# Optimization experiments

Measured on AMD Instinct MI355X. Metric: run time of the kernel, lower is better.

Reference implementation:

```python
import jax, jax.numpy as jnp
import numpy as np

B, S, D = 2, 2048, 2048
H, KVH, DH = 32, 8, 64
G = H // KVH  # num_key_value_groups
SCALE = DH ** -0.5
NEG = -1e9


def rotate_half(x):
    x1, x2 = jnp.split(x, 2, axis=-1)
    return jnp.concatenate([-x2, x1], axis=-1)


def setup_inputs() -> dict:
    key = jax.random.key(0)
    ks = jax.random.split(key, 6)
    hidden_states = jax.random.normal(ks[0], (B, S, D), dtype=jnp.float32)
    # RoPE tables (base 10000), shape [B, S, DH]
    inv_freq = 1.0 / (10000.0 ** (np.arange(0, DH, 2, dtype=np.float32) / DH))
    t = np.arange(S, dtype=np.float32)
    freqs = np.outer(t, inv_freq)                     # [S, DH/2]
    emb = np.concatenate([freqs, freqs], axis=-1)     # [S, DH]
    cos = jnp.broadcast_to(jnp.cos(emb)[None], (B, S, DH)).astype(jnp.float32)
    sin = jnp.broadcast_to(jnp.sin(emb)[None], (B, S, DH)).astype(jnp.float32)
    # additive causal mask [B, 1, S, S]
    causal = np.tril(np.ones((S, S), dtype=bool))
    mask = jnp.asarray(np.where(causal, 0.0, NEG).astype(np.float32))
    attention_mask = jnp.broadcast_to(mask[None, None], (B, 1, S, S))
    std = 0.02
    Wq = jax.random.normal(ks[1], (H * DH, D), dtype=jnp.float32) * std
    Wk = jax.random.normal(ks[2], (KVH * DH, D), dtype=jnp.float32) * std
    Wv = jax.random.normal(ks[3], (KVH * DH, D), dtype=jnp.float32) * std
    Wo = jax.random.normal(ks[4], (D, H * DH), dtype=jnp.float32) * std
    return {"hidden_states": hidden_states, "cos": cos, "sin": sin,
            "attention_mask": attention_mask, "Wq": Wq, "Wk": Wk, "Wv": Wv, "Wo": Wo}


def reference(hidden_states, cos, sin, attention_mask, Wq, Wk, Wv, Wo):
    b, s, d = hidden_states.shape
    # projections -> [B, heads, S, DH]
    q = (hidden_states @ Wq.T).reshape(b, s, H, DH).transpose(0, 2, 1, 3)
    k = (hidden_states @ Wk.T).reshape(b, s, KVH, DH).transpose(0, 2, 1, 3)
    v = (hidden_states @ Wv.T).reshape(b, s, KVH, DH).transpose(0, 2, 1, 3)
    # RoPE (unsqueeze_dim=1)
    c = cos[:, None]  # [B,1,S,DH]
    sn = sin[:, None]
    q = q * c + rotate_half(q) * sn
    k = k * c + rotate_half(k) * sn
    # GQA: repeat kv heads
    k = jnp.repeat(k, G, axis=1)
    v = jnp.repeat(v, G, axis=1)
    scores = jnp.einsum("bhqd,bhkd->bhqk", q, k) * SCALE + attention_mask
    attn = jax.nn.softmax(scores.astype(jnp.float32), axis=-1).astype(q.dtype)
    out = jnp.einsum("bhqk,bhkd->bhqd", attn, v)          # [B,H,S,DH]
    out = out.transpose(0, 2, 1, 3).reshape(b, s, H * DH)  # [B,S,H*DH]
    return out @ Wo.T
```

## Files before the change

kernel.cpp:

```cpp
#include <hip/hip_runtime.h>

typedef unsigned short u16;
typedef __attribute__((ext_vector_type(8))) short s16x8;
typedef __attribute__((ext_vector_type(4))) float f32x4;
typedef __attribute__((ext_vector_type(4))) unsigned short u16x4;

#define MFMA16(a, b, c) __builtin_amdgcn_mfma_f32_16x16x32_bf16(a, b, c, 0, 0, 0)

__device__ __forceinline__ u16 f2bf(float f) {
  unsigned u = __builtin_bit_cast(unsigned, f);
  u += 0x7fffu + ((u >> 16) & 1u);
  return (u16)(u >> 16);
}

__device__ __forceinline__ u16 f2bf_fast(float f) {
  return (u16)((__builtin_bit_cast(unsigned, f) + 0x8000u) >> 16);
}

__device__ __forceinline__ void async16(const void* g, void* l) {
  __builtin_amdgcn_global_load_lds(
      (const __attribute__((address_space(1))) void*)g,
      (__attribute__((address_space(3))) void*)l, 16, 0, 0);
}

__device__ __forceinline__ s16x8 ld8(const u16* p) { return *(const s16x8*)p; }

#define PRE 0.18033688011112042f

__global__ __launch_bounds__(256) void cvt_all(
    const float* __restrict__ X, const float* __restrict__ Wq,
    const float* __restrict__ Wk, const float* __restrict__ Wv,
    const float* __restrict__ Wo, u16* __restrict__ out) {
  long e = (long)(blockIdx.x * 256 + threadIdx.x) * 4;
  const float* src;
  if (e < 8388608L) src = X + e;
  else if (e < 12582912L) src = Wq + (e - 8388608L);
  else if (e < 13631488L) src = Wk + (e - 12582912L);
  else if (e < 14680064L) src = Wv + (e - 13631488L);
  else src = Wo + (e - 14680064L);
  float4 v = *(const float4*)src;
  u16x4 o = {f2bf(v.x), f2bf(v.y), f2bf(v.z), f2bf(v.w)};
  *(u16x4*)(out + e) = o;
}

enum { EPI_QKV = 0, EPI_OUT = 1 };

template <int EPI>
__global__ __launch_bounds__(256) void gemm_nt(
    const u16* __restrict__ A, const u16* __restrict__ Bm,
    const float* __restrict__ cosp, const float* __restrict__ sinp,
    u16* __restrict__ Qo, u16* __restrict__ Ko, u16* __restrict__ Vo,
    float* __restrict__ Co, int K) {
  __shared__ u16 SM[16384];
  const int t = threadIdx.x;
  const int lane = t & 63;
  const int w = t >> 6, wm = w >> 1, wn = w & 1;
  const int quad = lane >> 4, c16 = lane & 15;
  const int m0 = blockIdx.y * 128, n0 = blockIdx.x * 128;

  f32x4 acc[4][4];
  const f32x4 zero = {0.f, 0.f, 0.f, 0.f};
#pragma unroll
  for (int i = 0; i < 4; ++i)
#pragma unroll
    for (int j = 0; j < 4; ++j) acc[i][j] = zero;

  const u16* gA[4];
  const u16* gB[4];
#pragma unroll
  for (int p = 0; p < 4; ++p) {
    int c = t + p * 256;
    int r = c >> 3, cc = (c & 7) ^ (r & 7);
    gA[p] = A + (size_t)(m0 + r) * K + cc * 8;
    gB[p] = Bm + (size_t)(n0 + r) * K + cc * 8;
  }

  for (int k0 = 0; k0 < K; k0 += 64) {
    __syncthreads();
#pragma unroll
    for (int p = 0; p < 4; ++p) {
      async16(gA[p], &SM[(t + p * 256) * 8]);
      async16(gB[p], &SM[8192 + (t + p * 256) * 8]);
      gA[p] += 64;
      gB[p] += 64;
    }
    __syncthreads();
#pragma unroll
    for (int c = 0; c < 2; ++c) {
      s16x8 af[4], bfr[4];
#pragma unroll
      for (int i = 0; i < 4; ++i)
        af[i] = ld8(&SM[(wm * 64 + i * 16 + c16) * 64 +
                        (((c * 4 + quad) ^ (c16 & 7)) * 8)]);
#pragma unroll
      for (int j = 0; j < 4; ++j)
        bfr[j] = ld8(&SM[8192 + (wn * 64 + j * 16 + c16) * 64 +
                         (((c * 4 + quad) ^ (c16 & 7)) * 8)]);
#pragma unroll
      for (int i = 0; i < 4; ++i)
#pragma unroll
        for (int j = 0; j < 4; ++j) acc[i][j] = MFMA16(af[i], bfr[j], acc[i][j]);
    }
  }

  if (EPI == EPI_OUT) {
#pragma unroll
    for (int i = 0; i < 4; ++i)
#pragma unroll
      for (int r = 0; r < 4; ++r) {
        int m = m0 + wm * 64 + i * 16 + quad * 4 + r;
        float* dst = Co + (size_t)m * 2048 + n0 + wn * 64 + c16;
#pragma unroll
        for (int j = 0; j < 4; ++j) dst[j * 16] = acc[i][j][r];
      }
  } else if (n0 >= 2560) {
    __syncthreads();
#pragma unroll
    for (int i = 0; i < 4; ++i)
#pragma unroll
      for (int r = 0; r < 4; ++r) {
        int sl = wm * 64 + i * 16 + quad * 4 + r;
#pragma unroll
        for (int j = 0; j < 4; ++j) {
          int dl = wn * 64 + j * 16 + c16;
          SM[dl * 128 + (((sl >> 3) ^ (dl & 15)) * 8) + (sl & 7)] =
              f2bf(acc[i][j][r]);
        }
      }
    __syncthreads();
    int bb = m0 >> 11, m0s = m0 & 2047;
#pragma unroll
    for (int p = 0; p < 8; ++p) {
      int q = p * 256 + t;
      int dl = q >> 4, k = q & 15;
      s16x8 vrow = ld8(&SM[dl * 128 + ((k ^ (dl & 15)) * 8)]);
      int nab = n0 + dl;
      int kvh = (nab - 2560) >> 6, dh = nab & 63;
      *(s16x8*)(Vo + ((size_t)(bb * 8 + kvh) * 64 + dh) * 2048 + m0s + k * 8) =
          vrow;
    }
  } else {
    const int nbase = n0 + wn * 64;
#pragma unroll
    for (int i = 0; i < 4; ++i)
#pragma unroll
      for (int r = 0; r < 4; ++r) {
        int m = m0 + wm * 64 + i * 16 + quad * 4 + r;
        int b = m >> 11, s = m & 2047;
        if (nbase < 2048) {
          int h = nbase >> 6;
          size_t base = ((size_t)(b * 32 + h) * 2048 + s) * 64;
#pragma unroll
          for (int j = 0; j < 2; ++j) {
            int d = j * 16 + c16;
            float v1 = acc[i][j][r], v2 = acc[i][j + 2][r];
            float c1 = cosp[m * 64 + d], s1 = sinp[m * 64 + d];
            float c2 = cosp[m * 64 + d + 32], s2 = sinp[m * 64 + d + 32];
            Qo[base + d] = f2bf((v1 * c1 - v2 * s1) * PRE);
            Qo[base + d + 32] = f2bf((v2 * c2 + v1 * s2) * PRE);
          }
        } else {
          int h = (nbase - 2048) >> 6;
          size_t base = ((size_t)(b * 8 + h) * 2048 + s) * 64;
#pragma unroll
          for (int j = 0; j < 2; ++j) {
            int d = j * 16 + c16;
            float v1 = acc[i][j][r], v2 = acc[i][j + 2][r];
            float c1 = cosp[m * 64 + d], s1 = sinp[m * 64 + d];
            float c2 = cosp[m * 64 + d + 32], s2 = sinp[m * 64 + d + 32];
            Ko[base + d] = f2bf(v1 * c1 - v2 * s1);
            Ko[base + d + 32] = f2bf(v2 * c2 + v1 * s2);
          }
        }
      }
  }
}

__global__ __launch_bounds__(256) void attn(const u16* __restrict__ Q,
                                            const u16* __restrict__ Kg,
                                            const u16* __restrict__ Vg,
                                            u16* __restrict__ O) {
  __shared__ u16 Ks[2][4096];
  __shared__ u16 Vs[2][4096];
  __shared__ u16 Ps[8192];
  const int t = threadIdx.x;
  const int lane = t & 63;
  const int w = t >> 6;
  const int quad = lane >> 4, c16 = lane & 15;
  const int bh = blockIdx.y;
  const int b = bh >> 5, h = bh & 31;
  const int kvh = h >> 2;

  const u16* Qbase = Q + ((size_t)(b * 32 + h) * 2048) * 64;
  const u16* Kbase = Kg + ((size_t)(b * 8 + kvh) * 2048) * 64;
  const u16* Vbase = Vg + ((size_t)(b * 8 + kvh) * 64) * 2048;

  const int sr0 = t >> 3, sc0 = ((t & 7) ^ (sr0 & 7)) * 8;
  const int sr1 = (t + 256) >> 3, sc1 = (((t + 256) & 7) ^ (sr1 & 7)) * 8;

  for (int ph = 0; ph < 2; ++ph) {
    const int qt = ph ? 15 - blockIdx.x : blockIdx.x;
    const int q0 = qt * 128;

    s16x8 qa[2][2];
#pragma unroll
    for (int im = 0; im < 2; ++im)
#pragma unroll
      for (int c = 0; c < 2; ++c)
        qa[im][c] = ld8(Qbase + (size_t)(q0 + w * 32 + im * 16 + c16) * 64 +
                        c * 32 + quad * 8);

    f32x4 oacc[2][4];
    const f32x4 zero = {0.f, 0.f, 0.f, 0.f};
    float lacc[2][4];
#pragma unroll
    for (int im = 0; im < 2; ++im)
#pragma unroll
      for (int r = 0; r < 4; ++r) lacc[im][r] = 0.f;
#pragma unroll
    for (int im = 0; im < 2; ++im)
#pragma unroll
      for (int dt = 0; dt < 4; ++dt) oacc[im][dt] = zero;

    const int nkt = 2 * qt + 2;

    __syncthreads();
    {
      const u16* kg = Kbase + 0 * 4096;
      async16(kg + sr0 * 64 + sc0, &Ks[0][t * 8]);
      async16(kg + sr1 * 64 + sc1, &Ks[0][t * 8 + 2048]);
      async16(Vbase + (size_t)sr0 * 2048 + sc0, &Vs[0][t * 8]);
      async16(Vbase + (size_t)sr1 * 2048 + sc1, &Vs[0][t * 8 + 2048]);
    }

    for (int kt = 0; kt < nkt; ++kt) {
      const int cur = kt & 1;
      __syncthreads();
      if (kt + 1 < nkt) {
        const int nxt = 1 - cur;
        const u16* kg = Kbase + (kt + 1) * 4096;
        async16(kg + sr0 * 64 + sc0, &Ks[nxt][t * 8]);
        async16(kg + sr1 * 64 + sc1, &Ks[nxt][t * 8 + 2048]);
        async16(Vbase + (size_t)sr0 * 2048 + (kt + 1) * 64 + sc0,
                &Vs[nxt][t * 8]);
        async16(Vbase + (size_t)sr1 * 2048 + (kt + 1) * 64 + sc1,
                &Vs[nxt][t * 8 + 2048]);
      }
      const u16* Kb = Ks[cur];
      const u16* Vb = Vs[cur];

#pragma unroll
      for (int im = 0; im < 2; ++im) {
        f32x4 sc[4];
#pragma unroll
        for (int in = 0; in < 4; ++in) sc[in] = zero;
#pragma unroll
        for (int c = 0; c < 2; ++c)
#pragma unroll
          for (int in = 0; in < 4; ++in) {
            s16x8 kf = ld8(&Kb[(in * 16 + c16) * 64 +
                               (((c * 4 + quad) ^ (c16 & 7)) * 8)]);
            sc[in] = MFMA16(qa[im][c], kf, sc[in]);
          }
        const int rbase = q0 + w * 32 + im * 16;
        if (kt * 64 + 63 > rbase) {
#pragma unroll
          for (int in = 0; in < 4; ++in) {
            int kcol = kt * 64 + in * 16 + c16;
#pragma unroll
            for (int r = 0; r < 4; ++r)
              if (kcol > rbase + quad * 4 + r) sc[in][r] = -1e30f;
          }
        }
#pragma unroll
        for (int in = 0; in < 4; ++in)
#pragma unroll
          for (int r = 0; r < 4; ++r) {
            float p = exp2f(sc[in][r]);
            lacc[im][r] += p;
            int row = im * 16 + quad * 4 + r;
            Ps[w * 2048 + row * 64 +
               (((in * 2 + (c16 >> 3)) ^ (row & 7)) * 8) + (c16 & 7)] =
                f2bf_fast(p);
          }
      }

#pragma unroll
      for (int c = 0; c < 2; ++c) {
        const int swz = ((c * 4 + quad) ^ (c16 & 7)) * 8;
        s16x8 pf[2];
#pragma unroll
        for (int im = 0; im < 2; ++im)
          pf[im] = ld8(&Ps[w * 2048 + (im * 16 + c16) * 64 + swz]);
#pragma unroll
        for (int dt = 0; dt < 4; ++dt) {
          s16x8 vf = ld8(&Vb[(dt * 16 + c16) * 64 + swz]);
#pragma unroll
          for (int im = 0; im < 2; ++im)
            oacc[im][dt] = MFMA16(pf[im], vf, oacc[im][dt]);
        }
      }
    }

#pragma unroll
    for (int im = 0; im < 2; ++im) {
      float inv[4];
#pragma unroll
      for (int r = 0; r < 4; ++r) {
        float v = lacc[im][r];
        v += __shfl_xor(v, 1);
        v += __shfl_xor(v, 2);
        v += __shfl_xor(v, 4);
        v += __shfl_xor(v, 8);
        inv[r] = 1.f / v;
      }
#pragma unroll
      for (int dt = 0; dt < 4; ++dt)
#pragma unroll
        for (int r = 0; r < 4; ++r) {
          int s = q0 + w * 32 + im * 16 + quad * 4 + r;
          O[((size_t)(b * 2048 + s)) * 2048 + h * 64 + dt * 16 + c16] =
              f2bf(oacc[im][dt][r] * inv[r]);
        }
    }
  }
}

extern "C" void kernel_launch(void* const* d_in, const int* in_sizes, int n_in,
                              void* d_out, int out_size, void* d_ws,
                              size_t ws_size, hipStream_t stream) {
  const float* X = (const float*)d_in[0];
  const float* cosp = (const float*)d_in[1];
  const float* sinp = (const float*)d_in[2];
  const float* Wq = (const float*)d_in[4];
  const float* Wk = (const float*)d_in[5];
  const float* Wv = (const float*)d_in[6];
  const float* Wo = (const float*)d_in[7];
  float* out = (float*)d_out;

  u16* Xb = (u16*)d_ws;
  u16* Wqkv = Xb + 8388608;
  u16* Wob = Wqkv + 6291456;
  u16* Qr = Wob + 4194304;
  u16* Kr = Qr + 8388608;
  u16* Vt = Kr + 2097152;
  u16* Ob = Vt + 2097152;

  cvt_all<<<18432, 256, 0, stream>>>(X, Wq, Wk, Wv, Wo, Xb);

  gemm_nt<EPI_QKV><<<dim3(24, 32), 256, 0, stream>>>(
      Xb, Wqkv, cosp, sinp, Qr, Kr, Vt, nullptr, 2048);

  attn<<<dim3(8, 64), 256, 0, stream>>>(Qr, Kr, Vt, Ob);

  gemm_nt<EPI_OUT><<<dim3(16, 32), 256, 0, stream>>>(
      Ob, Wob, nullptr, nullptr, nullptr, nullptr, nullptr, out, 2048);
}
```

Before: 354.7 us.

## Double-buffer GEMM LDS tiles with K-step 32 and prefetch next tile

The projection GEMM main loop now uses two LDS buffers with a K-step of 32 instead of a single buffer with a K-step of 64. The global-to-LDS async load of the next tile is issued before the MFMAs on the current tile, which removes one barrier per iteration and overlaps load latency with compute. The LDS layout packs two rows per 64-element line with a new XOR swizzle, and the fragment offsets are precomputed. In exchange there are twice as many loop iterations, each with less compute to hide the loads behind.

```diff
diff --git a/kernel.cpp b/kernel.cpp
--- a/kernel.cpp
+++ b/kernel.cpp
@@ -65,42 +65,61 @@
 #pragma unroll
     for (int j = 0; j < 4; ++j) acc[i][j] = zero;
 
-  const u16* gA[4];
-  const u16* gB[4];
-#pragma unroll
-  for (int p = 0; p < 4; ++p) {
+  const u16* gA[2];
+  const u16* gB[2];
+  int lof[2];
+#pragma unroll
+  for (int p = 0; p < 2; ++p) {
     int c = t + p * 256;
-    int r = c >> 3, cc = (c & 7) ^ (r & 7);
-    gA[p] = A + (size_t)(m0 + r) * K + cc * 8;
-    gB[p] = Bm + (size_t)(n0 + r) * K + cc * 8;
-  }
-
-  for (int k0 = 0; k0 < K; k0 += 64) {
+    int dr = c >> 3, k8 = (c & 7) ^ (dr & 7);
+    int row = 2 * dr + (k8 >> 2), col = (k8 & 3) * 8;
+    gA[p] = A + (size_t)(m0 + row) * K + col;
+    gB[p] = Bm + (size_t)(n0 + row) * K + col;
+    lof[p] = c * 8;
+  }
+
+  int aoff[4], boff[4];
+#pragma unroll
+  for (int i = 0; i < 4; ++i) {
+    int rowA = wm * 64 + i * 16 + c16;
+    int drA = rowA >> 1;
+    int chA = (((rowA & 1) << 2) | quad) ^ (drA & 7);
+    aoff[i] = drA * 64 + chA * 8;
+    int rowB = wn * 64 + i * 16 + c16;
+    int drB = rowB >> 1;
+    int chB = (((rowB & 1) << 2) | quad) ^ (drB & 7);
+    boff[i] = 4096 + drB * 64 + chB * 8;
+  }
+
+#pragma unroll
+  for (int p = 0; p < 2; ++p) {
+    async16(gA[p], &SM[lof[p]]);
+    async16(gB[p], &SM[4096 + lof[p]]);
+  }
+
+  const int niter = K >> 5;
+  for (int kt = 0; kt < niter; ++kt) {
+    const int cb = (kt & 1) * 8192;
     __syncthreads();
-#pragma unroll
-    for (int p = 0; p < 4; ++p) {
-      async16(gA[p], &SM[(t + p * 256) * 8]);
-      async16(gB[p], &SM[8192 + (t + p * 256) * 8]);
-      gA[p] += 64;
-      gB[p] += 64;
-    }
-    __syncthreads();
-#pragma unroll
-    for (int c = 0; c < 2; ++c) {
-      s16x8 af[4], bfr[4];
-#pragma unroll
-      for (int i = 0; i < 4; ++i)
-        af[i] = ld8(&SM[(wm * 64 + i * 16 + c16) * 64 +
-                        (((c * 4 + quad) ^ (c16 & 7)) * 8)]);
-#pragma unroll
-      for (int j = 0; j < 4; ++j)
-        bfr[j] = ld8(&SM[8192 + (wn * 64 + j * 16 + c16) * 64 +
-                         (((c * 4 + quad) ^ (c16 & 7)) * 8)]);
-#pragma unroll
-      for (int i = 0; i < 4; ++i)
-#pragma unroll
-        for (int j = 0; j < 4; ++j) acc[i][j] = MFMA16(af[i], bfr[j], acc[i][j]);
-    }
+    if (kt + 1 < niter) {
+      const int nb = 8192 - cb;
+#pragma unroll
+      for (int p = 0; p < 2; ++p) {
+        gA[p] += 32;
+        gB[p] += 32;
+        async16(gA[p], &SM[nb + lof[p]]);
+        async16(gB[p], &SM[nb + 4096 + lof[p]]);
+      }
+    }
+    s16x8 af[4], bfr[4];
+#pragma unroll
+    for (int i = 0; i < 4; ++i) af[i] = ld8(&SM[cb + aoff[i]]);
+#pragma unroll
+    for (int j = 0; j < 4; ++j) bfr[j] = ld8(&SM[cb + boff[j]]);
+#pragma unroll
+    for (int i = 0; i < 4; ++i)
+#pragma unroll
+      for (int j = 0; j < 4; ++j) acc[i][j] = MFMA16(af[i], bfr[j], acc[i][j]);
   }
 
   if (EPI == EPI_OUT) {
@@ -226,7 +245,7 @@
 
     __syncthreads();
     {
-      const u16* kg = Kbase + 0 * 4096;
+      const u16* kg = Kbase;
       async16(kg + sr0 * 64 + sc0, &Ks[0][t * 8]);
       async16(kg + sr1 * 64 + sc1, &Ks[0][t * 8 + 2048]);
       async16(Vbase + (size_t)sr0 * 2048 + sc0, &Vs[0][t * 8]);
```

Result: faster. 328.7 us (-7.3%).
